# Kernel optimization log

Measured on AMD Instinct MI355X. Metric: run time of the kernel, lower is better.

The kernel has to match this reference:

```python
import jax, jax.numpy as jnp
import numpy as np

N = 50000          # nodes
E = 800000         # edges (avg degree 16)
F = 128            # in_dim = num_hidden*heads = pred_dim
H = 4              # attention heads per layer
D = 32             # num_hidden (per-head dim)
R = 11             # rel_num
L = 2              # num_layers
SCALE = float(1.0 / np.sqrt(D))


def setup_inputs() -> dict:
    key = jax.random.key(0)
    ks = jax.random.split(key, 16)
    inputs = jax.random.normal(ks[0], (N, F), jnp.float32)
    edge_types = jax.random.randint(ks[1], (E,), 0, R)
    src = jax.random.randint(ks[2], (E,), 0, N)
    dst = jax.random.randint(ks[3], (E,), 0, N)
    centrality = jax.random.uniform(ks[4], (N,), jnp.float32)
    rel_emb = jax.random.normal(ks[5], (R, F), jnp.float32) * 0.1
    # stacked per-layer projection weights (both layers have F -> H*D = F)
    Wq = jax.random.normal(ks[6], (L, F, H * D), jnp.float32) * 0.05
    Wk = jax.random.normal(ks[7], (L, F, H * D), jnp.float32) * 0.05
    Wv = jax.random.normal(ks[8], (L, F, H * D), jnp.float32) * 0.05
    We = jax.random.normal(ks[9], (L, F, H * D), jnp.float32) * 0.05
    bq = jnp.zeros((L, H * D), jnp.float32)
    bk = jnp.zeros((L, H * D), jnp.float32)
    bv = jnp.zeros((L, H * D), jnp.float32)
    be = jnp.zeros((L, H * D), jnp.float32)
    W_out = jax.random.normal(ks[10], (H * D, 1), jnp.float32) * 0.05
    b_out = jnp.zeros((1,), jnp.float32)
    gamma = jnp.ones((1,), jnp.float32)
    beta = jnp.zeros((1,), jnp.float32)
    return {"inputs": inputs, "edge_types": edge_types, "src": src, "dst": dst,
            "centrality": centrality, "rel_emb": rel_emb,
            "Wq": Wq, "bq": bq, "Wk": Wk, "bk": bk, "Wv": Wv, "bv": bv,
            "We": We, "be": be, "W_out": W_out, "b_out": b_out,
            "gamma": gamma, "beta": beta}


def _segment_softmax(score, dst, n):
    # score: [E, H]; softmax over incoming edges of each dst node
    m = jax.ops.segment_max(score, dst, num_segments=n)          # [N, H]
    ex = jnp.exp(score - m[dst])                                  # [E, H]
    s = jax.ops.segment_sum(ex, dst, num_segments=n)              # [N, H]
    return ex / (s[dst] + 1e-9)


def reference(inputs, edge_types, src, dst, centrality, rel_emb,
              Wq, bq, Wk, bk, Wv, bv, We, be, W_out, b_out, gamma, beta):
    h = inputs                                   # [N, F]
    ef = rel_emb[edge_types]                     # [E, pred_dim] relational edge embedding
    for l in range(L):
        q = (h @ Wq[l] + bq[l]).reshape(N, H, D)
        k = (h @ Wk[l] + bk[l]).reshape(N, H, D)
        v = (h @ Wv[l] + bv[l]).reshape(N, H, D)
        e = (ef @ We[l] + be[l]).reshape(E, H, D)
        # edge_mode="add": edge features added to keys/values on each edge
        ke = k[src] + e                           # [E, H, D]
        score = jnp.sum(q[dst] * ke, axis=-1) * SCALE   # [E, H]
        attn = _segment_softmax(score, dst, N)          # [E, H]
        msg = attn[:, :, None] * (v[src] + e)           # [E, H, D]
        agg = jax.ops.segment_sum(msg, dst, num_segments=N)  # [N, H, D]
        # identity residual (in_dim == H*D) + ELU activation
        h = jax.nn.elu(agg.reshape(N, H * D) + h)
    logits = h @ W_out + b_out                    # [N, 1]
    logits = jax.nn.relu((centrality * gamma + beta)[:, None] * logits)
    return logits
```

## Files before the change

kernel.cpp:

```cpp
#include <hip/hip_runtime.h>
#include <hip/hip_bf16.h>
#include <math.h>

#define SCALE_C 0.17677669529663687f
#define CAPP 64

typedef short bf16x8 __attribute__((ext_vector_type(8)));
typedef float f32x4 __attribute__((ext_vector_type(4)));


__global__ __launch_bounds__(256) void scatter_pad_k(
    const int* __restrict__ dst, const int* __restrict__ src, const int* __restrict__ etype,
    int E, int* __restrict__ cnt, int* __restrict__ bins) {
  int e = blockIdx.x * 256 + threadIdx.x;
  if (e < E) {
    int d = dst[e];
    int pos = atomicAdd(&cnt[d], 1);
    if (pos < CAPP) bins[(d << 6) + pos] = src[e] | (etype[e] << 20);
  }
}


__global__ __launch_bounds__(256) void prep_k(
    const float* __restrict__ Wq, const float* __restrict__ Wk, const float* __restrict__ Wv,
    __hip_bfloat16* __restrict__ wf,
    const float* __restrict__ rel_emb, const float* __restrict__ We, const float* __restrict__ be,
    float* __restrict__ re, int R) {
  int b = blockIdx.x;
  if (b < 48) {
    int tid = b * 256 + threadIdx.x;
    int lane = tid & 63;
    int frag = tid >> 6;
    int ks = frag & 3;
    int ct = (frag >> 2) & 7;
    int mat = frag >> 5;
    int l = mat / 3, m = mat % 3;
    const float* W = ((m == 0) ? Wq : (m == 1) ? Wk : Wv) + (size_t)l * 128 * 128;
    int nn = ct * 16 + (lane & 15);
    int k0 = ks * 32 + (lane >> 4) * 8;
    __hip_bfloat16 tmp[8];
    #pragma unroll
    for (int j = 0; j < 8; ++j) tmp[j] = __float2bfloat16(W[(size_t)(k0 + j) * 128 + nn]);
    *(uint4*)&wf[(size_t)frag * 64 * 8 + (size_t)lane * 8] = *(const uint4*)tmp;
  } else {
    int idx = (b - 48) * 256 + threadIdx.x;
    int tot = 2 * R * 128;
    if (idx >= tot) return;
    int c = idx & 127;
    int r = (idx >> 7) % R;
    int l = idx / (R * 128);
    const float* W = We + (size_t)l * 128 * 128;
    float acc = be[l * 128 + c];
    for (int kk = 0; kk < 128; ++kk) acc += rel_emb[r * 128 + kk] * W[kk * 128 + c];
    re[idx] = acc;
  }
}


__global__ __launch_bounds__(128) void qkv_k(
    const float* __restrict__ X, const __hip_bfloat16* __restrict__ wf,
    const float* __restrict__ bq, const float* __restrict__ bk, const float* __restrict__ bv,
    float* __restrict__ qo, __hip_bfloat16* __restrict__ kvo, int n) {
  __shared__ __hip_bfloat16 kvt[2][32][264];
  int wid = threadIdx.x >> 6;
  int lane = threadIdx.x & 63;
  int row0 = blockIdx.x * 64 + wid * 32;
  if (row0 >= n) return;
  int cl = lane & 15;
  int quad = lane >> 4;

  bf16x8 afrag[2][4];
  #pragma unroll
  for (int s = 0; s < 2; ++s) {
    int arow = row0 + s * 16 + cl;
    bool av = arow < n;
    const float* xr = X + (size_t)arow * 128 + quad * 8;
    #pragma unroll
    for (int ks = 0; ks < 4; ++ks) {
      float4 x0 = av ? *(const float4*)(xr + ks * 32)     : make_float4(0.f, 0.f, 0.f, 0.f);
      float4 x1 = av ? *(const float4*)(xr + ks * 32 + 4) : make_float4(0.f, 0.f, 0.f, 0.f);
      union { bf16x8 v; __hip_bfloat16 h[8]; } fu;
      fu.h[0] = __float2bfloat16(x0.x); fu.h[1] = __float2bfloat16(x0.y);
      fu.h[2] = __float2bfloat16(x0.z); fu.h[3] = __float2bfloat16(x0.w);
      fu.h[4] = __float2bfloat16(x1.x); fu.h[5] = __float2bfloat16(x1.y);
      fu.h[6] = __float2bfloat16(x1.z); fu.h[7] = __float2bfloat16(x1.w);
      afrag[s][ks] = fu.v;
    }
  }
  const uint4* wfu = (const uint4*)wf;

  #pragma unroll
  for (int ct = 0; ct < 8; ++ct) {
    f32x4 a0 = {0.f, 0.f, 0.f, 0.f}, a1 = {0.f, 0.f, 0.f, 0.f};
    #pragma unroll
    for (int ks = 0; ks < 4; ++ks) {
      uint4 braw = wfu[((size_t)ct * 4 + ks) * 64 + lane];
      bf16x8 bfr = __builtin_bit_cast(bf16x8, braw);
      a0 = __builtin_amdgcn_mfma_f32_16x16x32_bf16(afrag[0][ks], bfr, a0, 0, 0, 0);
      a1 = __builtin_amdgcn_mfma_f32_16x16x32_bf16(afrag[1][ks], bfr, a1, 0, 0, 0);
    }
    int c = ct * 16 + cl;
    float bb = bq[c];
    #pragma unroll
    for (int r = 0; r < 4; ++r) {
      int row = row0 + quad * 4 + r;
      if (row < n) qo[(size_t)row * 128 + c] = a0[r] + bb;
      if (row + 16 < n) qo[(size_t)(row + 16) * 128 + c] = a1[r] + bb;
    }
  }

  #pragma unroll
  for (int m = 1; m <= 2; ++m) {
    const float* bias = (m == 1) ? bk : bv;
    #pragma unroll
    for (int ct = 0; ct < 8; ++ct) {
      f32x4 a0 = {0.f, 0.f, 0.f, 0.f}, a1 = {0.f, 0.f, 0.f, 0.f};
      #pragma unroll
      for (int ks = 0; ks < 4; ++ks) {
        uint4 braw = wfu[((size_t)(m * 8 + ct) * 4 + ks) * 64 + lane];
        bf16x8 bfr = __builtin_bit_cast(bf16x8, braw);
        a0 = __builtin_amdgcn_mfma_f32_16x16x32_bf16(afrag[0][ks], bfr, a0, 0, 0, 0);
        a1 = __builtin_amdgcn_mfma_f32_16x16x32_bf16(afrag[1][ks], bfr, a1, 0, 0, 0);
      }
      int c = ct * 16 + cl;
      float bb = bias[c];
      int p = 8 * (c >> 2) + (c & 3) + ((m == 2) ? 4 : 0);
      #pragma unroll
      for (int r = 0; r < 4; ++r) {
        kvt[wid][quad * 4 + r][p]      = __float2bfloat16(a0[r] + bb);
        kvt[wid][16 + quad * 4 + r][p] = __float2bfloat16(a1[r] + bb);
      }
    }
  }

  const uint4* tsrc = (const uint4*)&kvt[wid][0][0];
  #pragma unroll
  for (int it = 0; it < 16; ++it) {
    int idx = it * 64 + lane;
    int row = idx >> 5, off = idx & 31;
    if (row0 + row < n)
      *(uint4*)&kvo[((size_t)(row0 + row)) * 256 + off * 8] = tsrc[row * 33 + off];
  }
}


__global__ __launch_bounds__(256) void edge_k(
    const float* __restrict__ q, const __hip_bfloat16* __restrict__ kv,
    const float* __restrict__ re,
    const int* __restrict__ bins, const int* __restrict__ cnt,
    const float* __restrict__ h_in, float* __restrict__ h_out,
    const float* __restrict__ Wout, const float* __restrict__ bout,
    const float* __restrict__ cent, const float* __restrict__ gamma,
    const float* __restrict__ beta, float* __restrict__ outp, int n) {
  int node = blockIdx.x * 4 + (threadIdx.x >> 6);
  if (node >= n) return;
  int lane = threadIdx.x & 63;
  int j = lane & 15;
  int quarter = lane >> 4;
  int rs = node << 6;
  int deg = cnt[node];
  deg = deg < CAPP ? deg : CAPP;

  const float4* qrow = (const float4*)q + ((uint)node * 32u + (uint)(j * 2));
  float4 qa = qrow[0], qb = qrow[1];
  qa.x *= SCALE_C; qa.y *= SCALE_C; qa.z *= SCALE_C; qa.w *= SCALE_C;
  qb.x *= SCALE_C; qb.y *= SCALE_C; qb.z *= SCALE_C; qb.w *= SCALE_C;

  float ssum = 0.f;
  float acc0 = 0.f, acc1 = 0.f, acc2 = 0.f, acc3 = 0.f;
  float acc4 = 0.f, acc5 = 0.f, acc6 = 0.f, acc7 = 0.f;
  int nit = (deg + 3) >> 2;
  int pk = (quarter < deg) ? bins[rs + quarter] : 0;
  for (int i = 0; i < nit; ++i) {
    int eidx = 4 * i + quarter;
    bool valid = eidx < deg;
    uint s_ = (uint)pk & 0xFFFFFu;
    uint t_ = (uint)pk >> 20;
    int en = eidx + 4;
    int pk_n = (en < deg) ? bins[rs + en] : 0;
    const uint4* kr = (const uint4*)kv + (s_ * 32u + (uint)(j * 2));
    uint4 raw0 = kr[0];
    uint4 raw1 = kr[1];
    const float4* rr = (const float4*)re + (t_ * 32u + (uint)(j * 2));
    float4 r0 = rr[0];
    float4 r1 = rr[1];
    float k0 = __uint_as_float(raw0.x << 16);
    float k1 = __uint_as_float(raw0.x & 0xffff0000u);
    float k2 = __uint_as_float(raw0.y << 16);
    float k3 = __uint_as_float(raw0.y & 0xffff0000u);
    float v0 = __uint_as_float(raw0.z << 16);
    float v1 = __uint_as_float(raw0.z & 0xffff0000u);
    float v2 = __uint_as_float(raw0.w << 16);
    float v3 = __uint_as_float(raw0.w & 0xffff0000u);
    float k4 = __uint_as_float(raw1.x << 16);
    float k5 = __uint_as_float(raw1.x & 0xffff0000u);
    float k6 = __uint_as_float(raw1.y << 16);
    float k7 = __uint_as_float(raw1.y & 0xffff0000u);
    float v4 = __uint_as_float(raw1.z << 16);
    float v5 = __uint_as_float(raw1.z & 0xffff0000u);
    float v6 = __uint_as_float(raw1.w << 16);
    float v7 = __uint_as_float(raw1.w & 0xffff0000u);
    float p = qa.x * (k0 + r0.x) + qa.y * (k1 + r0.y) + qa.z * (k2 + r0.z) + qa.w * (k3 + r0.w)
            + qb.x * (k4 + r1.x) + qb.y * (k5 + r1.y) + qb.z * (k6 + r1.z) + qb.w * (k7 + r1.w);
    p += __shfl_xor(p, 1);
    p += __shfl_xor(p, 2);
    float w = valid ? __expf(p) : 0.f;
    ssum += w;
    acc0 += w * (v0 + r0.x);
    acc1 += w * (v1 + r0.y);
    acc2 += w * (v2 + r0.z);
    acc3 += w * (v3 + r0.w);
    acc4 += w * (v4 + r1.x);
    acc5 += w * (v5 + r1.y);
    acc6 += w * (v6 + r1.z);
    acc7 += w * (v7 + r1.w);
    pk = pk_n;
  }
  ssum += __shfl_xor(ssum, 16); ssum += __shfl_xor(ssum, 32);
  acc0 += __shfl_xor(acc0, 16); acc0 += __shfl_xor(acc0, 32);
  acc1 += __shfl_xor(acc1, 16); acc1 += __shfl_xor(acc1, 32);
  acc2 += __shfl_xor(acc2, 16); acc2 += __shfl_xor(acc2, 32);
  acc3 += __shfl_xor(acc3, 16); acc3 += __shfl_xor(acc3, 32);
  acc4 += __shfl_xor(acc4, 16); acc4 += __shfl_xor(acc4, 32);
  acc5 += __shfl_xor(acc5, 16); acc5 += __shfl_xor(acc5, 32);
  acc6 += __shfl_xor(acc6, 16); acc6 += __shfl_xor(acc6, 32);
  acc7 += __shfl_xor(acc7, 16); acc7 += __shfl_xor(acc7, 32);
  if (quarter != 0) return;

  float inv = 1.f / (ssum + 1e-9f);
  const float4* hrow = (const float4*)h_in + ((uint)node * 32u + (uint)(j * 2));
  float4 h0 = hrow[0], h1 = hrow[1];
  float x0 = acc0 * inv + h0.x;
  float x1 = acc1 * inv + h0.y;
  float x2 = acc2 * inv + h0.z;
  float x3 = acc3 * inv + h0.w;
  float x4 = acc4 * inv + h1.x;
  float x5 = acc5 * inv + h1.y;
  float x6 = acc6 * inv + h1.z;
  float x7 = acc7 * inv + h1.w;
  x0 = x0 > 0.f ? x0 : expm1f(x0);
  x1 = x1 > 0.f ? x1 : expm1f(x1);
  x2 = x2 > 0.f ? x2 : expm1f(x2);
  x3 = x3 > 0.f ? x3 : expm1f(x3);
  x4 = x4 > 0.f ? x4 : expm1f(x4);
  x5 = x5 > 0.f ? x5 : expm1f(x5);
  x6 = x6 > 0.f ? x6 : expm1f(x6);
  x7 = x7 > 0.f ? x7 : expm1f(x7);
  if (outp == nullptr) {
    float4* orow = (float4*)h_out + ((uint)node * 32u + (uint)(j * 2));
    orow[0] = make_float4(x0, x1, x2, x3);
    orow[1] = make_float4(x4, x5, x6, x7);
  } else {
    const float4* wrow = (const float4*)Wout + (uint)(j * 2);
    float4 w0 = wrow[0], w1 = wrow[1];
    float pp = x0 * w0.x + x1 * w0.y + x2 * w0.z + x3 * w0.w
             + x4 * w1.x + x5 * w1.y + x6 * w1.z + x7 * w1.w;
    pp += __shfl_xor(pp, 1);
    pp += __shfl_xor(pp, 2);
    pp += __shfl_xor(pp, 4);
    pp += __shfl_xor(pp, 8);
    if (lane == 0) {
      float lg = pp + bout[0];
      lg *= (cent[node] * gamma[0] + beta[0]);
      outp[node] = fmaxf(lg, 0.f);
    }
  }
}


extern "C" void kernel_launch(void* const* d_in, const int* in_sizes, int n_in,
                              void* d_out, int out_size, void* d_ws, size_t ws_size,
                              hipStream_t stream) {
  const float* inputs  = (const float*)d_in[0];
  const int*   etype   = (const int*)d_in[1];
  const int*   src     = (const int*)d_in[2];
  const int*   dst     = (const int*)d_in[3];
  const float* cent    = (const float*)d_in[4];
  const float* rel_emb = (const float*)d_in[5];
  const float* Wq      = (const float*)d_in[6];
  const float* bq      = (const float*)d_in[7];
  const float* Wk      = (const float*)d_in[8];
  const float* bk      = (const float*)d_in[9];
  const float* Wv      = (const float*)d_in[10];
  const float* bv      = (const float*)d_in[11];
  const float* We      = (const float*)d_in[12];
  const float* be      = (const float*)d_in[13];
  const float* Wout    = (const float*)d_in[14];
  const float* bout    = (const float*)d_in[15];
  const float* gamma   = (const float*)d_in[16];
  const float* beta    = (const float*)d_in[17];
  float* out = (float*)d_out;

  const int N = in_sizes[0] / 128;
  const int E = in_sizes[1];
  const int R = in_sizes[5] / 128;

  float* fw   = (float*)d_ws;
  float* q    = fw;
  float* hbuf = q + (size_t)N * 128;
  float* re   = hbuf + (size_t)N * 128;
  __hip_bfloat16* kv = (__hip_bfloat16*)(re + 2 * (size_t)R * 128);
  __hip_bfloat16* wf = kv + (size_t)N * 256;
  int* cnt  = (int*)(wf + 6 * 16384);
  int* bins = cnt + N;

  hipMemsetAsync(cnt, 0, (size_t)N * sizeof(int), stream);

  int ebl = (E + 255) / 256;
  scatter_pad_k<<<ebl, 256, 0, stream>>>(dst, src, etype, E, cnt, bins);
  prep_k<<<48 + (2 * R * 128 + 255) / 256, 256, 0, stream>>>(Wq, Wk, Wv, wf, rel_emb, We, be, re, R);

  int qb = (N + 63) / 64;
  int eb = (N + 3) / 4;
  for (int l = 0; l < 2; ++l) {
    const float* X = (l == 0) ? inputs : hbuf;
    size_t bo = (size_t)l * 128;
    qkv_k<<<qb, 128, 0, stream>>>(X, wf + (size_t)l * 3 * 16384,
                                  bq + bo, bk + bo, bv + bo, q, kv, N);
    edge_k<<<eb, 256, 0, stream>>>(q, kv, re + (size_t)l * R * 128, bins, cnt,
                                   X, hbuf, Wout, bout, cent, gamma, beta,
                                   (l == 1) ? out : nullptr, N);
  }
}
```

Measured before the change: 323.0 us.

## Store Q as pre-scaled bf16, prefetch edge gathers, fold count memset into prep

The QKV kernel now writes Q as bf16 with the attention scale folded in, staged through shared memory for coalesced stores. This halves Q traffic and removes the scaling in the edge kernel. The edge kernel double-buffers the neighbor K/V and relation-embedding gathers one iteration ahead to hide gather latency, at the cost of more registers. The count-buffer memset is merged into the prep kernel to drop an API call. Lower Q precision slightly changes the attention scores.

New measurement: 310.0 us. 1.04x faster.

```diff
diff --git a/kernel.cpp b/kernel.cpp
--- a/kernel.cpp
+++ b/kernel.cpp
@@ -25,7 +25,7 @@
     const float* __restrict__ Wq, const float* __restrict__ Wk, const float* __restrict__ Wv,
     __hip_bfloat16* __restrict__ wf,
     const float* __restrict__ rel_emb, const float* __restrict__ We, const float* __restrict__ be,
-    float* __restrict__ re, int R) {
+    float* __restrict__ re, int R, int* __restrict__ cnt, int N, int reb) {
   int b = blockIdx.x;
   if (b < 48) {
     int tid = b * 256 + threadIdx.x;
@@ -42,7 +42,7 @@
     #pragma unroll
     for (int j = 0; j < 8; ++j) tmp[j] = __float2bfloat16(W[(size_t)(k0 + j) * 128 + nn]);
     *(uint4*)&wf[(size_t)frag * 64 * 8 + (size_t)lane * 8] = *(const uint4*)tmp;
-  } else {
+  } else if (b < 48 + reb) {
     int idx = (b - 48) * 256 + threadIdx.x;
     int tot = 2 * R * 128;
     if (idx >= tot) return;
@@ -53,6 +53,11 @@
     float acc = be[l * 128 + c];
     for (int kk = 0; kk < 128; ++kk) acc += rel_emb[r * 128 + kk] * W[kk * 128 + c];
     re[idx] = acc;
+  } else {
+    int idx = (b - 48 - reb) * 256 + threadIdx.x;
+    int nq = N >> 2;
+    if (idx < nq) ((uint4*)cnt)[idx] = make_uint4(0, 0, 0, 0);
+    if (idx == nq) for (int k = nq << 2; k < N; ++k) cnt[k] = 0;
   }
 }
 
@@ -60,7 +65,7 @@
 __global__ __launch_bounds__(128) void qkv_k(
     const float* __restrict__ X, const __hip_bfloat16* __restrict__ wf,
     const float* __restrict__ bq, const float* __restrict__ bk, const float* __restrict__ bv,
-    float* __restrict__ qo, __hip_bfloat16* __restrict__ kvo, int n) {
+    __hip_bfloat16* __restrict__ qo, __hip_bfloat16* __restrict__ kvo, int n) {
   __shared__ __hip_bfloat16 kvt[2][32][264];
   int wid = threadIdx.x >> 6;
   int lane = threadIdx.x & 63;
@@ -103,9 +108,18 @@
     float bb = bq[c];
     #pragma unroll
     for (int r = 0; r < 4; ++r) {
-      int row = row0 + quad * 4 + r;
-      if (row < n) qo[(size_t)row * 128 + c] = a0[r] + bb;
-      if (row + 16 < n) qo[(size_t)(row + 16) * 128 + c] = a1[r] + bb;
+      kvt[wid][quad * 4 + r][c]      = __float2bfloat16((a0[r] + bb) * SCALE_C);
+      kvt[wid][16 + quad * 4 + r][c] = __float2bfloat16((a1[r] + bb) * SCALE_C);
+    }
+  }
+  {
+    const uint4* tsrc = (const uint4*)&kvt[wid][0][0];
+    #pragma unroll
+    for (int it = 0; it < 8; ++it) {
+      int idx = it * 64 + lane;
+      int row = idx >> 4, g = idx & 15;
+      if (row0 + row < n)
+        *(uint4*)&qo[((size_t)(row0 + row)) * 128 + g * 8] = tsrc[row * 33 + g];
     }
   }
 
@@ -132,20 +146,21 @@
       }
     }
   }
-
-  const uint4* tsrc = (const uint4*)&kvt[wid][0][0];
-  #pragma unroll
-  for (int it = 0; it < 16; ++it) {
-    int idx = it * 64 + lane;
-    int row = idx >> 5, off = idx & 31;
-    if (row0 + row < n)
-      *(uint4*)&kvo[((size_t)(row0 + row)) * 256 + off * 8] = tsrc[row * 33 + off];
+  {
+    const uint4* tsrc = (const uint4*)&kvt[wid][0][0];
+    #pragma unroll
+    for (int it = 0; it < 16; ++it) {
+      int idx = it * 64 + lane;
+      int row = idx >> 5, off = idx & 31;
+      if (row0 + row < n)
+        *(uint4*)&kvo[((size_t)(row0 + row)) * 256 + off * 8] = tsrc[row * 33 + off];
+    }
   }
 }
 
 
 __global__ __launch_bounds__(256) void edge_k(
-    const float* __restrict__ q, const __hip_bfloat16* __restrict__ kv,
+    const __hip_bfloat16* __restrict__ qb, const __hip_bfloat16* __restrict__ kv,
     const float* __restrict__ re,
     const int* __restrict__ bins, const int* __restrict__ cnt,
     const float* __restrict__ h_in, float* __restrict__ h_out,
@@ -161,29 +176,40 @@
   int deg = cnt[node];
   deg = deg < CAPP ? deg : CAPP;
 
-  const float4* qrow = (const float4*)q + ((uint)node * 32u + (uint)(j * 2));
-  float4 qa = qrow[0], qb = qrow[1];
-  qa.x *= SCALE_C; qa.y *= SCALE_C; qa.z *= SCALE_C; qa.w *= SCALE_C;
-  qb.x *= SCALE_C; qb.y *= SCALE_C; qb.z *= SCALE_C; qb.w *= SCALE_C;
+  uint4 qraw = *((const uint4*)(qb + ((size_t)node << 7)) + j);
+  float qa0 = __uint_as_float(qraw.x << 16), qa1 = __uint_as_float(qraw.x & 0xffff0000u);
+  float qa2 = __uint_as_float(qraw.y << 16), qa3 = __uint_as_float(qraw.y & 0xffff0000u);
+  float qa4 = __uint_as_float(qraw.z << 16), qa5 = __uint_as_float(qraw.z & 0xffff0000u);
+  float qa6 = __uint_as_float(qraw.w << 16), qa7 = __uint_as_float(qraw.w & 0xffff0000u);
 
   float ssum = 0.f;
   float acc0 = 0.f, acc1 = 0.f, acc2 = 0.f, acc3 = 0.f;
   float acc4 = 0.f, acc5 = 0.f, acc6 = 0.f, acc7 = 0.f;
   int nit = (deg + 3) >> 2;
-  int pk = (quarter < deg) ? bins[rs + quarter] : 0;
+
+  int pk1 = (quarter < deg) ? bins[rs + quarter] : 0;
+  int pk2 = (quarter + 4 < deg) ? bins[rs + quarter + 4] : 0;
+  uint s0 = (uint)pk1 & 0xFFFFFu, t0 = (uint)pk1 >> 20;
+  const uint4* kr0 = (const uint4*)kv + (s0 * 32u + (uint)(j * 2));
+  uint4 raw0 = kr0[0];
+  uint4 raw1 = kr0[1];
+  const float4* rr0 = (const float4*)re + (t0 * 32u + (uint)(j * 2));
+  float4 r0 = rr0[0];
+  float4 r1 = rr0[1];
+  pk1 = pk2;
+
   for (int i = 0; i < nit; ++i) {
-    int eidx = 4 * i + quarter;
-    bool valid = eidx < deg;
-    uint s_ = (uint)pk & 0xFFFFFu;
-    uint t_ = (uint)pk >> 20;
-    int en = eidx + 4;
-    int pk_n = (en < deg) ? bins[rs + en] : 0;
-    const uint4* kr = (const uint4*)kv + (s_ * 32u + (uint)(j * 2));
-    uint4 raw0 = kr[0];
-    uint4 raw1 = kr[1];
-    const float4* rr = (const float4*)re + (t_ * 32u + (uint)(j * 2));
-    float4 r0 = rr[0];
-    float4 r1 = rr[1];
+    int e2 = 4 * (i + 2) + quarter;
+    pk2 = (e2 < deg) ? bins[rs + e2] : 0;
+    uint s1 = (uint)pk1 & 0xFFFFFu, t1 = (uint)pk1 >> 20;
+    const uint4* krn = (const uint4*)kv + (s1 * 32u + (uint)(j * 2));
+    uint4 nraw0 = krn[0];
+    uint4 nraw1 = krn[1];
+    const float4* rrn = (const float4*)re + (t1 * 32u + (uint)(j * 2));
+    float4 nr0 = rrn[0];
+    float4 nr1 = rrn[1];
+
+    bool valid = 4 * i + quarter < deg;
     float k0 = __uint_as_float(raw0.x << 16);
     float k1 = __uint_as_float(raw0.x & 0xffff0000u);
     float k2 = __uint_as_float(raw0.y << 16);
@@ -200,8 +226,8 @@
     float v5 = __uint_as_float(raw1.z & 0xffff0000u);
     float v6 = __uint_as_float(raw1.w << 16);
     float v7 = __uint_as_float(raw1.w & 0xffff0000u);
-    float p = qa.x * (k0 + r0.x) + qa.y * (k1 + r0.y) + qa.z * (k2 + r0.z) + qa.w * (k3 + r0.w)
-            + qb.x * (k4 + r1.x) + qb.y * (k5 + r1.y) + qb.z * (k6 + r1.z) + qb.w * (k7 + r1.w);
+    float p = qa0 * (k0 + r0.x) + qa1 * (k1 + r0.y) + qa2 * (k2 + r0.z) + qa3 * (k3 + r0.w)
+            + qa4 * (k4 + r1.x) + qa5 * (k5 + r1.y) + qa6 * (k6 + r1.z) + qa7 * (k7 + r1.w);
     p += __shfl_xor(p, 1);
     p += __shfl_xor(p, 2);
     float w = valid ? __expf(p) : 0.f;
@@ -214,7 +240,9 @@
     acc5 += w * (v5 + r1.y);
     acc6 += w * (v6 + r1.z);
     acc7 += w * (v7 + r1.w);
-    pk = pk_n;
+
+    raw0 = nraw0; raw1 = nraw1; r0 = nr0; r1 = nr1;
+    pk1 = pk2;
   }
   ssum += __shfl_xor(ssum, 16); ssum += __shfl_xor(ssum, 32);
   acc0 += __shfl_xor(acc0, 16); acc0 += __shfl_xor(acc0, 32);
@@ -296,28 +324,28 @@
   const int R = in_sizes[5] / 128;
 
   float* fw   = (float*)d_ws;
-  float* q    = fw;
-  float* hbuf = q + (size_t)N * 128;
+  float* hbuf = fw;
   float* re   = hbuf + (size_t)N * 128;
-  __hip_bfloat16* kv = (__hip_bfloat16*)(re + 2 * (size_t)R * 128);
+  __hip_bfloat16* qb = (__hip_bfloat16*)(re + 2 * (size_t)R * 128);
+  __hip_bfloat16* kv = qb + (size_t)N * 128;
   __hip_bfloat16* wf = kv + (size_t)N * 256;
   int* cnt  = (int*)(wf + 6 * 16384);
   int* bins = cnt + N;
 
-  hipMemsetAsync(cnt, 0, (size_t)N * sizeof(int), stream);
-
+  int reb = (2 * R * 128 + 255) / 256;
+  int zb  = (N / 4 + 256) / 256;
+  prep_k<<<48 + reb + zb, 256, 0, stream>>>(Wq, Wk, Wv, wf, rel_emb, We, be, re, R, cnt, N, reb);
   int ebl = (E + 255) / 256;
   scatter_pad_k<<<ebl, 256, 0, stream>>>(dst, src, etype, E, cnt, bins);
-  prep_k<<<48 + (2 * R * 128 + 255) / 256, 256, 0, stream>>>(Wq, Wk, Wv, wf, rel_emb, We, be, re, R);
-
-  int qb = (N + 63) / 64;
+
+  int qbks = (N + 63) / 64;
   int eb = (N + 3) / 4;
   for (int l = 0; l < 2; ++l) {
     const float* X = (l == 0) ? inputs : hbuf;
     size_t bo = (size_t)l * 128;
-    qkv_k<<<qb, 128, 0, stream>>>(X, wf + (size_t)l * 3 * 16384,
-                                  bq + bo, bk + bo, bv + bo, q, kv, N);
-    edge_k<<<eb, 256, 0, stream>>>(q, kv, re + (size_t)l * R * 128, bins, cnt,
+    qkv_k<<<qbks, 128, 0, stream>>>(X, wf + (size_t)l * 3 * 16384,
+                                    bq + bo, bk + bo, bv + bo, qb, kv, N);
+    edge_k<<<eb, 256, 0, stream>>>(qb, kv, re + (size_t)l * R * 128, bins, cnt,
                                    X, hbuf, Wout, bout, cent, gamma, beta,
                                    (l == 1) ? out : nullptr, N);
   }
```
